# Kernel optimization log

Hardware: AMD Instinct MI355X
Metric: run time of the kernel (lower is better)

Reference implementation:

```python
import jax, jax.numpy as jnp
import numpy as np

B, L, D, P = 8, 2048, 1024, 4  # batch, length, word_dim, phrase_len


def setup_inputs() -> dict:
    key = jax.random.key(0)
    kx, kw, kb = jax.random.split(key, 3)
    x = jax.random.normal(kx, (B, L, D), dtype=jnp.float32)
    # torch nn.Linear(phrase_dim, word_dim): W [out=D, in=D*P], b [D]
    scale = 1.0 / np.sqrt(D * P)
    W = jax.random.uniform(kw, (D, D * P), dtype=jnp.float32, minval=-scale, maxval=scale)
    b = jax.random.uniform(kb, (D,), dtype=jnp.float32, minval=-scale, maxval=scale)
    return {"x": x, "W": W, "b": b}


def reference(x, W, b):
    Bs, Ls, Ds = x.shape
    Ps = W.shape[1] // Ds  # phrase_len
    # gram[i][:, t] = x[:, t - i] (zero for t < i): left-pad by i, keep first L steps.
    # Stack on the LAST axis then reshape, matching torch's contiguous view over
    # (dim, phrase_len) -> feature index d*P + i.
    grams = jnp.stack(
        [jnp.pad(x, ((0, 0), (i, 0), (0, 0)))[:, :Ls, :] for i in range(Ps)],
        axis=-1,
    )  # [B, L, D, P]
    feat = grams.reshape(Bs, Ls, Ds * Ps)  # [B, L, D*P]
    # nn.Linear: y = feat @ W.T + b
    return jnp.einsum("blf,df->bld", feat, W) + b
```

## Files before the change

### kernel.cpp

```cpp
#include <hip/hip_runtime.h>
#include <hip/hip_bf16.h>
#include <stdint.h>

#define Bq 8
#define Lq 2048
#define Dq 1024
#define Pq 4
#define Kq 4096
#define LPAD 2056
#define BM 256
#define BN 256
#define BK 64

typedef __attribute__((ext_vector_type(8))) short short8;
typedef __attribute__((ext_vector_type(4))) float f32x4;

__device__ __forceinline__ unsigned short f2bf(float f) {
  unsigned u = __float_as_uint(f);
  u += 0x7FFFu + ((u >> 16) & 1u);
  return (unsigned short)(u >> 16);
}

__device__ __forceinline__ void gload_lds16(const void* g, void* l) {
  __builtin_amdgcn_global_load_lds(
      (const __attribute__((address_space(1))) void*)g,
      (__attribute__((address_space(3))) void*)l, 16, 0, 0);
}

__global__ void k_prep(const float* __restrict__ x, const float* __restrict__ W,
                       unsigned short* __restrict__ xp, unsigned short* __restrict__ Wp) {
  if (blockIdx.x < 8224u) {
    unsigned g = blockIdx.x * blockDim.x + threadIdx.x;
    unsigned base = g * 8;
    const unsigned total = (unsigned)Bq * LPAD * Dq;
    if (base >= total) return;
    unsigned t = base >> 10;
    unsigned b = t / LPAD;
    unsigned r = t - b * LPAD;
    unsigned d = base & 1023;
    short8 o;
    if (r >= 3 && r < 3 + Lq) {
      const float* s = x + ((size_t)b * Lq + (r - 3)) * Dq + d;
      float4 v0 = *(const float4*)(s);
      float4 v1 = *(const float4*)(s + 4);
      o[0] = (short)f2bf(v0.x); o[1] = (short)f2bf(v0.y);
      o[2] = (short)f2bf(v0.z); o[3] = (short)f2bf(v0.w);
      o[4] = (short)f2bf(v1.x); o[5] = (short)f2bf(v1.y);
      o[6] = (short)f2bf(v1.z); o[7] = (short)f2bf(v1.w);
    } else {
      o = (short8)0;
    }
    *(short8*)(xp + base) = o;
  } else {
    unsigned g = (blockIdx.x - 8224u) * blockDim.x + threadIdx.x;
    unsigned base = g * 8;
    unsigned d = base >> 12;
    unsigned rem = base & 4095;
    unsigned dp = rem >> 2;
    const float4* src = (const float4*)(W + base);
    float4 v0 = src[0];
    float4 v1 = src[1];
    float a0[4] = {v0.x, v0.y, v0.z, v0.w};
    float a1[4] = {v1.x, v1.y, v1.z, v1.w};
#pragma unroll
    for (int i = 0; i < 4; ++i) {
      unsigned packed = (unsigned)f2bf(a0[i]) | ((unsigned)f2bf(a1[i]) << 16);
      *(unsigned*)(Wp + (size_t)d * 4096 + (size_t)i * 1024 + dp) = packed;
    }
  }
}


#define VM16 asm volatile("s_waitcnt vmcnt(16)" ::: "memory")
#define VM0  asm volatile("s_waitcnt vmcnt(0)"  ::: "memory")
#define BAR  __builtin_amdgcn_s_barrier()

#define STAGE(buf, kt) do { \
    const unsigned sclA_ = (((unsigned)(bRow0 - ((kt) >> 4))) << 11) + (((unsigned)(kt) & 15u) << 7); \
    const unsigned sclB_ = nScl + ((unsigned)(kt) << 7); \
    _Pragma("unroll") for (int j_ = 0; j_ < 8; ++j_) \
      gload_lds16((const char*)xp + (thrA + (unsigned)(j_ * 16384) + sclA_), \
                  lds + ((buf) << 15) + (wBase + (j_ << 10))); \
    _Pragma("unroll") for (int j_ = 0; j_ < 8; ++j_) \
      gload_lds16((const char*)Wp + (thrB + (unsigned)(j_ * 65536) + sclB_), \
                  lds + 65536 + ((buf) << 15) + (wBase + (j_ << 10))); \
  } while (0)

#define RD_SET(SA, SB, buf, kk) do { \
    _Pragma("unroll") for (int mi_ = 0; mi_ < 8; ++mi_) \
      SA[mi_] = *(const short8*)(lds + ((buf) << 15) + (mi_ << 11) + aK[kk]); \
    _Pragma("unroll") for (int ni_ = 0; ni_ < 8; ++ni_) \
      SB[ni_] = *(const short8*)(lds + ((buf) << 15) + (ni_ << 11) + bK[kk]); \
  } while (0)

#define MFMA_SET(SA, SB) do { \
    __builtin_amdgcn_s_setprio(1); \
    _Pragma("unroll") for (int mi_ = 0; mi_ < 8; ++mi_) \
    _Pragma("unroll") for (int ni_ = 0; ni_ < 8; ++ni_) \
      acc[mi_][ni_] = __builtin_amdgcn_mfma_f32_16x16x32_bf16( \
          SA[mi_], SB[ni_], acc[mi_][ni_], 0, 0, 0); \
    __builtin_amdgcn_s_setprio(0); \
  } while (0)

__global__ void __launch_bounds__(256, 1)
k_gemm(const unsigned short* __restrict__ xp,
       const unsigned short* __restrict__ Wp,
       const float* __restrict__ bias,
       float* __restrict__ out) {
  __shared__ __attribute__((aligned(16))) unsigned char lds[131072];

  const int tid  = threadIdx.x;
  const int lane = tid & 63;
  const int w    = tid >> 6;
  const int wm   = w >> 1;
  const int wn   = w & 1;

  const int bid = blockIdx.x;
  const int swz = (bid & 7) * 32 + (bid >> 3);
  const int m0 = (swz >> 2) * BM;
  const int n0 = (swz & 3) * BN;
  const int b  = m0 >> 11;
  const int l0 = m0 & 2047;
  const int bRow0 = b * LPAD + l0 + 3;
  const unsigned nScl = (unsigned)n0 << 13;

  const unsigned rowT = (unsigned)(64 * w + ((tid >> 3) & 7));
  const unsigned chnk = ((unsigned)((tid & 7) ^ ((tid >> 3) & 7))) << 4;
  const unsigned thrA = (rowT << 11) + chnk;
  const unsigned thrB = (rowT << 13) + chnk;
  const unsigned wBase = ((unsigned)w << 13) + ((unsigned)lane << 4);

  unsigned aK[2], bK[2];
  {
#pragma unroll
    for (int kk = 0; kk < 2; ++kk) {
      const int cb = (kk * 64 + ((lane >> 4) << 4)) ^ ((lane & 7) << 4);
      aK[kk] = (unsigned)(((wm * 128 + (lane & 15)) << 7) + cb);
      bK[kk] = (unsigned)(65536 + ((wn * 128 + (lane & 15)) << 7) + cb);
    }
  }

  f32x4 acc[8][8] = {};
  short8 s0a[8], s0b[8], s1a[8], s1b[8];

  STAGE(0, 0);
  STAGE(1, 1);
  VM16;
  BAR;
  RD_SET(s0a, s0b, 0, 0);

#pragma unroll 1
  for (int it = 0; it < 31; ++it) {
    const int T = it * 2;
    RD_SET(s1a, s1b, 0, 1);
    MFMA_SET(s0a, s0b);
    BAR;
    STAGE(0, T + 2);
    VM16; BAR;
    RD_SET(s0a, s0b, 1, 0);
    MFMA_SET(s1a, s1b);
    RD_SET(s1a, s1b, 1, 1);
    MFMA_SET(s0a, s0b);
    BAR;
    STAGE(1, T + 3);
    VM16; BAR;
    RD_SET(s0a, s0b, 0, 0);
    MFMA_SET(s1a, s1b);
  }

  RD_SET(s1a, s1b, 0, 1);
  MFMA_SET(s0a, s0b);
  BAR;
  VM0; BAR;
  RD_SET(s0a, s0b, 1, 0);
  MFMA_SET(s1a, s1b);
  RD_SET(s1a, s1b, 1, 1);
  MFMA_SET(s0a, s0b);
  MFMA_SET(s1a, s1b);

#pragma unroll
  for (int ni = 0; ni < 8; ++ni) {
    const int col = n0 + wn * 128 + ni * 16 + (lane & 15);
    const float bv = bias[col];
#pragma unroll
    for (int mi = 0; mi < 8; ++mi) {
      const int row0 = m0 + wm * 128 + mi * 16 + ((lane >> 4) << 2);
#pragma unroll
      for (int t2 = 0; t2 < 4; ++t2)
        out[(size_t)(row0 + t2) * Dq + col] = acc[mi][ni][t2] + bv;
    }
  }
}

__global__ void k_naive(const float* __restrict__ x, const float* __restrict__ W,
                        const float* __restrict__ bias, float* __restrict__ out) {
  size_t g = (size_t)blockIdx.x * blockDim.x + threadIdx.x;
  const size_t total = (size_t)Bq * Lq * Dq;
  if (g >= total) return;
  int d = (int)(g & 1023);
  int l = (int)((g >> 10) & 2047);
  int b = (int)(g >> 21);
  float s = bias[d];
  for (int i = 0; i < Pq; ++i) {
    if (l - i < 0) continue;
    const float* xr = x + ((size_t)b * Lq + (l - i)) * Dq;
    const float* wr = W + (size_t)d * Kq + i;
    float accv = 0.f;
    for (int dp = 0; dp < Dq; ++dp) accv += xr[dp] * wr[(size_t)dp * 4];
    s += accv;
  }
  out[g] = s;
}

extern "C" void kernel_launch(void* const* d_in, const int* in_sizes, int n_in,
                              void* d_out, int out_size, void* d_ws, size_t ws_size,
                              hipStream_t stream) {
  const float* x    = (const float*)d_in[0];
  const float* W    = (const float*)d_in[1];
  const float* bias = (const float*)d_in[2];
  float* out = (float*)d_out;

  const size_t WP_BYTES = (size_t)Dq * Kq * sizeof(unsigned short);
  const size_t XP_BYTES = (size_t)Bq * LPAD * Dq * sizeof(unsigned short);

  if (ws_size < WP_BYTES + XP_BYTES) {
    const size_t total = (size_t)Bq * Lq * Dq;
    k_naive<<<(unsigned)((total + 255) / 256), 256, 0, stream>>>(x, W, bias, out);
    return;
  }

  unsigned short* Wp = (unsigned short*)d_ws;
  unsigned short* xp = (unsigned short*)((char*)d_ws + WP_BYTES);

  k_prep<<<10272, 256, 0, stream>>>(x, W, xp, Wp);
  k_gemm<<<dim3((Bq * Lq / BM) * (Dq / BN)), 256, 0, stream>>>(xp, Wp, bias, out);
}
```

Baseline: 155.9 us.

## Shrink GEMM tile to 256x128x32 with triple-buffered LDS and two blocks per CU

The GEMM tile shrinks from 256x256 with K-step 64 to 256x128 with K-step 32. The K pipeline changes from double-buffered, paired register sets to a three-stage LDS ring in which each phase issues the next loads before running its MFMAs. Launch bounds move to two blocks per CU, LDS drops to 72KB, and the grid doubles with a new block swizzle. The aim is to raise occupancy and hide latency, at the cost of lower arithmetic intensity per tile, more barriers, and more global traffic for re-reading x and W.

Measured after the change: 152.0 us. 2.5% less time.

```diff
diff --git a/kernel.cpp b/kernel.cpp
--- a/kernel.cpp
+++ b/kernel.cpp
@@ -9,8 +9,8 @@
 #define Kq 4096
 #define LPAD 2056
 #define BM 256
-#define BN 256
-#define BK 64
+#define BN 128
+#define BK 32
 
 typedef __attribute__((ext_vector_type(8))) short short8;
 typedef __attribute__((ext_vector_type(4))) float f32x4;
@@ -71,43 +71,47 @@
 }
 
 
-#define VM16 asm volatile("s_waitcnt vmcnt(16)" ::: "memory")
-#define VM0  asm volatile("s_waitcnt vmcnt(0)"  ::: "memory")
-#define BAR  __builtin_amdgcn_s_barrier()
-
-#define STAGE(buf, kt) do { \
-    const unsigned sclA_ = (((unsigned)(bRow0 - ((kt) >> 4))) << 11) + (((unsigned)(kt) & 15u) << 7); \
-    const unsigned sclB_ = nScl + ((unsigned)(kt) << 7); \
-    _Pragma("unroll") for (int j_ = 0; j_ < 8; ++j_) \
-      gload_lds16((const char*)xp + (thrA + (unsigned)(j_ * 16384) + sclA_), \
-                  lds + ((buf) << 15) + (wBase + (j_ << 10))); \
-    _Pragma("unroll") for (int j_ = 0; j_ < 8; ++j_) \
-      gload_lds16((const char*)Wp + (thrB + (unsigned)(j_ * 65536) + sclB_), \
-                  lds + 65536 + ((buf) << 15) + (wBase + (j_ << 10))); \
-  } while (0)
-
-#define RD_SET(SA, SB, buf, kk) do { \
+#define VM6 asm volatile("s_waitcnt vmcnt(6)" ::: "memory")
+#define VM0 asm volatile("s_waitcnt vmcnt(0)" ::: "memory")
+#define BAR __builtin_amdgcn_s_barrier()
+
+#define STAGE_AB(AIMM, BIMM, kt) do { \
+    const unsigned sclA_ = (((unsigned)(bRow0 - ((kt) >> 5))) << 11) + (((unsigned)(kt) & 31u) << 6); \
+    const unsigned sclB_ = nScl + ((unsigned)(kt) << 6); \
+    _Pragma("unroll") for (int j_ = 0; j_ < 4; ++j_) \
+      gload_lds16((const char*)xp + (thrA + (unsigned)(j_ * 131072) + sclA_), \
+                  lds + (AIMM) + (j_ << 12) + (tid << 4)); \
+    _Pragma("unroll") for (int j_ = 0; j_ < 2; ++j_) \
+      gload_lds16((const char*)Wp + (thrB + (unsigned)(j_ * 524288) + sclB_), \
+                  lds + (BIMM) + (j_ << 12) + (tid << 4)); \
+  } while (0)
+
+#define READS(AIMM, BIMM) do { \
     _Pragma("unroll") for (int mi_ = 0; mi_ < 8; ++mi_) \
-      SA[mi_] = *(const short8*)(lds + ((buf) << 15) + (mi_ << 11) + aK[kk]); \
-    _Pragma("unroll") for (int ni_ = 0; ni_ < 8; ++ni_) \
-      SB[ni_] = *(const short8*)(lds + ((buf) << 15) + (ni_ << 11) + bK[kk]); \
-  } while (0)
-
-#define MFMA_SET(SA, SB) do { \
+      fa[mi_] = *(const short8*)(lds + aVG[mi_] + (AIMM)); \
+    _Pragma("unroll") for (int ni_ = 0; ni_ < 4; ++ni_) \
+      fb[ni_] = *(const short8*)(lds + bVG[ni_] + (BIMM)); \
+  } while (0)
+
+#define MFMA32 do { \
     __builtin_amdgcn_s_setprio(1); \
     _Pragma("unroll") for (int mi_ = 0; mi_ < 8; ++mi_) \
-    _Pragma("unroll") for (int ni_ = 0; ni_ < 8; ++ni_) \
+    _Pragma("unroll") for (int ni_ = 0; ni_ < 4; ++ni_) \
       acc[mi_][ni_] = __builtin_amdgcn_mfma_f32_16x16x32_bf16( \
-          SA[mi_], SB[ni_], acc[mi_][ni_], 0, 0, 0); \
+          fa[mi_], fb[ni_], acc[mi_][ni_], 0, 0, 0); \
     __builtin_amdgcn_s_setprio(0); \
   } while (0)
 
-__global__ void __launch_bounds__(256, 1)
+#define PHASE(AR, BR, AS, BS, kt) do { \
+    READS(AR, BR); STAGE_AB(AS, BS, kt); MFMA32; VM6; BAR; \
+  } while (0)
+
+__global__ void __launch_bounds__(256, 2)
 k_gemm(const unsigned short* __restrict__ xp,
        const unsigned short* __restrict__ Wp,
        const float* __restrict__ bias,
        float* __restrict__ out) {
-  __shared__ __attribute__((aligned(16))) unsigned char lds[131072];
+  __shared__ __attribute__((aligned(16))) unsigned char lds[73728];
 
   const int tid  = threadIdx.x;
   const int lane = tid & 63;
@@ -116,71 +120,54 @@
   const int wn   = w & 1;
 
   const int bid = blockIdx.x;
-  const int swz = (bid & 7) * 32 + (bid >> 3);
-  const int m0 = (swz >> 2) * BM;
-  const int n0 = (swz & 3) * BN;
+  const int swz = (bid & 7) * 64 + (bid >> 3);
+  const int m0 = (swz >> 3) * BM;
+  const int n0 = (swz & 7) * BN;
   const int b  = m0 >> 11;
   const int l0 = m0 & 2047;
   const int bRow0 = b * LPAD + l0 + 3;
   const unsigned nScl = (unsigned)n0 << 13;
 
-  const unsigned rowT = (unsigned)(64 * w + ((tid >> 3) & 7));
-  const unsigned chnk = ((unsigned)((tid & 7) ^ ((tid >> 3) & 7))) << 4;
-  const unsigned thrA = (rowT << 11) + chnk;
-  const unsigned thrB = (rowT << 13) + chnk;
-  const unsigned wBase = ((unsigned)w << 13) + ((unsigned)lane << 4);
-
-  unsigned aK[2], bK[2];
-  {
-#pragma unroll
-    for (int kk = 0; kk < 2; ++kk) {
-      const int cb = (kk * 64 + ((lane >> 4) << 4)) ^ ((lane & 7) << 4);
-      aK[kk] = (unsigned)(((wm * 128 + (lane & 15)) << 7) + cb);
-      bK[kk] = (unsigned)(65536 + ((wn * 128 + (lane & 15)) << 7) + cb);
-    }
-  }
-
-  f32x4 acc[8][8] = {};
-  short8 s0a[8], s0b[8], s1a[8], s1b[8];
-
-  STAGE(0, 0);
-  STAGE(1, 1);
-  VM16;
+  const unsigned rS   = (unsigned)(tid >> 2);
+  const unsigned clS  = (unsigned)((tid & 3) ^ ((tid >> 3) & 3));
+  const unsigned thrA = (rS << 11) + (clS << 4);
+  const unsigned thrB = (rS << 13) + (clS << 4);
+
+  const int r4 = lane & 15;
+  const int chunk = ((lane >> 4) ^ ((r4 >> 1) & 3)) << 4;
+  unsigned aVG[8], bVG[4];
+#pragma unroll
+  for (int mi = 0; mi < 8; ++mi)
+    aVG[mi] = (unsigned)(((wm * 128 + mi * 16 + r4) << 6) + chunk);
+#pragma unroll
+  for (int ni = 0; ni < 4; ++ni)
+    bVG[ni] = (unsigned)(((wn * 64 + ni * 16 + r4) << 6) + chunk);
+
+  f32x4 acc[8][4] = {};
+  short8 fa[8], fb[4];
+
+  STAGE_AB(24576, 0, 0);
+  STAGE_AB(40960, 8192, 1);
+  VM6;
   BAR;
-  RD_SET(s0a, s0b, 0, 0);
 
 #pragma unroll 1
-  for (int it = 0; it < 31; ++it) {
-    const int T = it * 2;
-    RD_SET(s1a, s1b, 0, 1);
-    MFMA_SET(s0a, s0b);
-    BAR;
-    STAGE(0, T + 2);
-    VM16; BAR;
-    RD_SET(s0a, s0b, 1, 0);
-    MFMA_SET(s1a, s1b);
-    RD_SET(s1a, s1b, 1, 1);
-    MFMA_SET(s0a, s0b);
-    BAR;
-    STAGE(1, T + 3);
-    VM16; BAR;
-    RD_SET(s0a, s0b, 0, 0);
-    MFMA_SET(s1a, s1b);
-  }
-
-  RD_SET(s1a, s1b, 0, 1);
-  MFMA_SET(s0a, s0b);
-  BAR;
+  for (int it = 0; it < 42; ++it) {
+    const int k0 = it * 3;
+    PHASE(24576, 0,     57344, 16384, k0 + 2);
+    PHASE(40960, 8192,  24576, 0,     k0 + 3);
+    PHASE(57344, 16384, 40960, 8192,  k0 + 4);
+  }
+
+  READS(24576, 0);
+  MFMA32;
   VM0; BAR;
-  RD_SET(s0a, s0b, 1, 0);
-  MFMA_SET(s1a, s1b);
-  RD_SET(s1a, s1b, 1, 1);
-  MFMA_SET(s0a, s0b);
-  MFMA_SET(s1a, s1b);
-
-#pragma unroll
-  for (int ni = 0; ni < 8; ++ni) {
-    const int col = n0 + wn * 128 + ni * 16 + (lane & 15);
+  READS(40960, 8192);
+  MFMA32;
+
+#pragma unroll
+  for (int ni = 0; ni < 4; ++ni) {
+    const int col = n0 + wn * 64 + ni * 16 + r4;
     const float bv = bias[col];
 #pragma unroll
     for (int mi = 0; mi < 8; ++mi) {
```
